# Kernel optimization log

Measured on AMD Instinct MI355X. Metric: run time of the kernel, lower is better.

The kernel has to match this reference:

```python
import jax, jax.numpy as jnp
import numpy as np

THRESH = 0.5
TAU = 0.5
GAMMA = 1.0
BETA = 0.9
A = 0.5
B = 0.5


def zif_spike(v):
    # ZIF surrogate: forward is hard threshold (v > 0).
    return (v > 0).astype(v.dtype)


def setup_inputs() -> dict:
    key = jax.random.key(0)
    x = jax.random.normal(key, (64, 8192, 100), dtype=jnp.float32)
    return {"x": x}


def reference(x):
    # x: [B, N, T]; scan over time with (mem, w) state kept per element.
    xt = jnp.moveaxis(x, 2, 0)  # [T, B, N]
    init_mem = jnp.zeros(xt.shape[1:], dtype=x.dtype)
    init_w = jnp.zeros(xt.shape[1:], dtype=x.dtype)

    def step(carry, x_t):
        mem, w = carry
        mem = mem * TAU + x_t - w
        spike = zif_spike(mem - THRESH)
        w = BETA * w + (1.0 - BETA) * (A * mem + B * spike)
        mem = mem - spike * THRESH  # soft reset
        return (mem, w), spike

    _, spikes = jax.lax.scan(step, (init_mem, init_w), xt)  # [T, B, N]
    return jnp.moveaxis(spikes, 0, 2)  # [B, N, T]
```

## Files before the change

### kernel.cpp

```cpp
#include <hip/hip_runtime.h>

#define T_STEPS 100
#define CHUNKS  25
#define TPB     64
#define ELEMS   64
#define PGRID   1536

typedef const __attribute__((address_space(1))) unsigned int g_u32;
typedef __attribute__((address_space(3))) unsigned int l_u32;

__global__ __launch_bounds__(TPB) void lif_kernel(const float* __restrict__ x,
                                                  float* __restrict__ out,
                                                  int nt) {
#pragma clang fp contract(off)
    __shared__ float4 tile[ELEMS * CHUNKS];

    const int lane = threadIdx.x;
    int ti = blockIdx.x;
    if (ti >= nt) return;

    {
        const float4* __restrict__ xb = (const float4*)x + (size_t)ti * (ELEMS * CHUNKS);
#pragma unroll
        for (int k = 0; k < CHUNKS; ++k) {
            __builtin_amdgcn_global_load_lds(
                (g_u32*)(xb + k * TPB + lane), (l_u32*)&tile[k * TPB], 16, 0, 0);
        }
    }
    asm volatile("s_waitcnt vmcnt(0)" ::: "memory");
    __builtin_amdgcn_sched_barrier(0);

    while (true) {
        float4 xv[CHUNKS];
#pragma unroll
        for (int c = 0; c < CHUNKS; ++c) xv[c] = tile[lane * CHUNKS + c];
        asm volatile("s_waitcnt lgkmcnt(0)" ::: "memory");
        __builtin_amdgcn_sched_barrier(0);

        const int nxt = ti + PGRID;
        if (nxt < nt) {
            const float4* __restrict__ xb = (const float4*)x + (size_t)nxt * (ELEMS * CHUNKS);
#pragma unroll
            for (int k = 0; k < CHUNKS; ++k) {
                __builtin_amdgcn_global_load_lds(
                    (g_u32*)(xb + k * TPB + lane), (l_u32*)&tile[k * TPB], 16, 0, 0);
            }
        }

        unsigned b0 = 0, b1 = 0, b2 = 0, b3 = 0;
        float mem = 0.0f, w = 0.0f;
#pragma unroll
        for (int c = 0; c < CHUNKS; ++c) {
            float xs[4] = {xv[c].x, xv[c].y, xv[c].z, xv[c].w};
#pragma unroll
            for (int j = 0; j < 4; ++j) {
                mem = (mem * 0.5f + xs[j]) - w;
                const bool fire = (mem - 0.5f) > 0.0f;
                const float spike = fire ? 1.0f : 0.0f;
                w = 0.9f * w + 0.1f * (0.5f * mem + 0.5f * spike);
                mem = mem - spike * 0.5f;
                const int t = c * 4 + j;
                const unsigned bit = fire ? 1u : 0u;
                if (t < 32)      b0 |= bit << t;
                else if (t < 64) b1 |= bit << (t - 32);
                else if (t < 96) b2 |= bit << (t - 64);
                else             b3 |= bit << (t - 96);
            }
        }

        float4* __restrict__ ob = (float4*)out + (size_t)ti * (ELEMS * CHUNKS);
#pragma unroll
        for (int k = 0; k < CHUNKS; ++k) {
            const int f = k * TPB + lane;
            const int e = f / 25;
            const int c = f - e * 25;
            const int a = e << 2;
            const unsigned w0 = (unsigned)__builtin_amdgcn_ds_bpermute(a, (int)b0);
            const unsigned w1 = (unsigned)__builtin_amdgcn_ds_bpermute(a, (int)b1);
            const unsigned w2 = (unsigned)__builtin_amdgcn_ds_bpermute(a, (int)b2);
            const unsigned w3 = (unsigned)__builtin_amdgcn_ds_bpermute(a, (int)b3);
            const unsigned word = (c < 16) ? ((c < 8) ? w0 : w1)
                                           : ((c < 24) ? w2 : w3);
            const int sh = (c & 7) * 4;
            float4 s;
            s.x = ((word >> (sh + 0)) & 1u) ? 1.0f : 0.0f;
            s.y = ((word >> (sh + 1)) & 1u) ? 1.0f : 0.0f;
            s.z = ((word >> (sh + 2)) & 1u) ? 1.0f : 0.0f;
            s.w = ((word >> (sh + 3)) & 1u) ? 1.0f : 0.0f;
            ob[f] = s;
        }

        ti = nxt;
        if (ti >= nt) break;
        asm volatile("s_waitcnt vmcnt(25)" ::: "memory");
        __builtin_amdgcn_sched_barrier(0);
    }
}

extern "C" void kernel_launch(void* const* d_in, const int* in_sizes, int n_in,
                              void* d_out, int out_size, void* d_ws, size_t ws_size,
                              hipStream_t stream) {
    const float* x = (const float*)d_in[0];
    float* out = (float*)d_out;
    int n_elem = in_sizes[0] / T_STEPS;
    int nt = n_elem / ELEMS;
    int grid = nt < PGRID ? nt : PGRID;

    lif_kernel<<<grid, TPB, 0, stream>>>(x, out, nt);
}
```

Before: 361.8 us.

## Switch to non-persistent 256-thread blocks with double-buffered time-slice loads

Replaces the persistent 64-thread grid, which prefetched whole 64-element tiles, with one 256-thread block per 256 elements. Each wave streams its 64 elements' time series in five 20-step slices through double-buffered LDS. The scan on one slice runs while the next slice loads, and LDS per block drops from a full tile to two small slice buffers. The cost is a much larger grid, no cross-tile prefetch, and strided 16-byte global gathers per slice instead of contiguous tile loads.

Measured after the change: 358.8 us. About the same (-0.8%).

```diff
diff --git a/kernel.cpp b/kernel.cpp
--- a/kernel.cpp
+++ b/kernel.cpp
@@ -2,64 +2,75 @@
 
 #define T_STEPS 100
 #define CHUNKS  25
-#define TPB     64
-#define ELEMS   64
-#define PGRID   1536
+#define TPB     256
+#define EPB     256
+#define SLICES  5
+#define SF4     5
+#define WSLOT   (64 * SF4)
 
 typedef const __attribute__((address_space(1))) unsigned int g_u32;
 typedef __attribute__((address_space(3))) unsigned int l_u32;
 
 __global__ __launch_bounds__(TPB) void lif_kernel(const float* __restrict__ x,
-                                                  float* __restrict__ out,
-                                                  int nt) {
+                                                  float* __restrict__ out) {
 #pragma clang fp contract(off)
-    __shared__ float4 tile[ELEMS * CHUNKS];
+    __shared__ float4 lds[2][EPB * SF4];
 
-    const int lane = threadIdx.x;
-    int ti = blockIdx.x;
-    if (ti >= nt) return;
+    const int tid  = threadIdx.x;
+    const int lane = tid & 63;
+    const int w    = tid >> 6;
 
-    {
-        const float4* __restrict__ xb = (const float4*)x + (size_t)ti * (ELEMS * CHUNKS);
+    const float* __restrict__ xw =
+        x + ((size_t)blockIdx.x * EPB + (size_t)w * 64) * T_STEPS;
+
+    const float* src[SF4];
 #pragma unroll
-        for (int k = 0; k < CHUNKS; ++k) {
-            __builtin_amdgcn_global_load_lds(
-                (g_u32*)(xb + k * TPB + lane), (l_u32*)&tile[k * TPB], 16, 0, 0);
+    for (int i = 0; i < SF4; ++i) {
+        const int f = i * 64 + lane;
+        const int e = f / SF4;
+        const int c = f - e * SF4;
+        src[i] = xw + e * T_STEPS + c * 4;
+    }
+
+#pragma unroll
+    for (int i = 0; i < SF4; ++i)
+        __builtin_amdgcn_global_load_lds(
+            (g_u32*)src[i], (l_u32*)&lds[0][w * WSLOT + i * 64], 16, 0, 0);
+
+    unsigned b0 = 0, b1 = 0, b2 = 0, b3 = 0;
+    float mem = 0.0f, wreg = 0.0f;
+
+#pragma unroll
+    for (int s = 0; s < SLICES; ++s) {
+        const int buf = s & 1;
+
+        if (s + 1 < SLICES) {
+#pragma unroll
+            for (int i = 0; i < SF4; ++i)
+                __builtin_amdgcn_global_load_lds(
+                    (g_u32*)(src[i] + (s + 1) * 4 * SF4),
+                    (l_u32*)&lds[buf ^ 1][w * WSLOT + i * 64], 16, 0, 0);
+            asm volatile("s_waitcnt vmcnt(5)" ::: "memory");
+        } else {
+            asm volatile("s_waitcnt vmcnt(0)" ::: "memory");
         }
-    }
-    asm volatile("s_waitcnt vmcnt(0)" ::: "memory");
-    __builtin_amdgcn_sched_barrier(0);
-
-    while (true) {
-        float4 xv[CHUNKS];
-#pragma unroll
-        for (int c = 0; c < CHUNKS; ++c) xv[c] = tile[lane * CHUNKS + c];
-        asm volatile("s_waitcnt lgkmcnt(0)" ::: "memory");
         __builtin_amdgcn_sched_barrier(0);
 
-        const int nxt = ti + PGRID;
-        if (nxt < nt) {
-            const float4* __restrict__ xb = (const float4*)x + (size_t)nxt * (ELEMS * CHUNKS);
+        float4 xv[SF4];
 #pragma unroll
-            for (int k = 0; k < CHUNKS; ++k) {
-                __builtin_amdgcn_global_load_lds(
-                    (g_u32*)(xb + k * TPB + lane), (l_u32*)&tile[k * TPB], 16, 0, 0);
-            }
-        }
+        for (int c = 0; c < SF4; ++c) xv[c] = lds[buf][tid * SF4 + c];
 
-        unsigned b0 = 0, b1 = 0, b2 = 0, b3 = 0;
-        float mem = 0.0f, w = 0.0f;
 #pragma unroll
-        for (int c = 0; c < CHUNKS; ++c) {
+        for (int c = 0; c < SF4; ++c) {
             float xs[4] = {xv[c].x, xv[c].y, xv[c].z, xv[c].w};
 #pragma unroll
             for (int j = 0; j < 4; ++j) {
-                mem = (mem * 0.5f + xs[j]) - w;
+                mem = (mem * 0.5f + xs[j]) - wreg;
                 const bool fire = (mem - 0.5f) > 0.0f;
                 const float spike = fire ? 1.0f : 0.0f;
-                w = 0.9f * w + 0.1f * (0.5f * mem + 0.5f * spike);
+                wreg = 0.9f * wreg + 0.1f * (0.5f * mem + 0.5f * spike);
                 mem = mem - spike * 0.5f;
-                const int t = c * 4 + j;
+                const int t = s * 20 + c * 4 + j;
                 const unsigned bit = fire ? 1u : 0u;
                 if (t < 32)      b0 |= bit << t;
                 else if (t < 64) b1 |= bit << (t - 32);
@@ -67,33 +78,29 @@
                 else             b3 |= bit << (t - 96);
             }
         }
+    }
 
-        float4* __restrict__ ob = (float4*)out + (size_t)ti * (ELEMS * CHUNKS);
+    float4* __restrict__ ow =
+        (float4*)out + ((size_t)blockIdx.x * EPB + (size_t)w * 64) * CHUNKS;
 #pragma unroll
-        for (int k = 0; k < CHUNKS; ++k) {
-            const int f = k * TPB + lane;
-            const int e = f / 25;
-            const int c = f - e * 25;
-            const int a = e << 2;
-            const unsigned w0 = (unsigned)__builtin_amdgcn_ds_bpermute(a, (int)b0);
-            const unsigned w1 = (unsigned)__builtin_amdgcn_ds_bpermute(a, (int)b1);
-            const unsigned w2 = (unsigned)__builtin_amdgcn_ds_bpermute(a, (int)b2);
-            const unsigned w3 = (unsigned)__builtin_amdgcn_ds_bpermute(a, (int)b3);
-            const unsigned word = (c < 16) ? ((c < 8) ? w0 : w1)
-                                           : ((c < 24) ? w2 : w3);
-            const int sh = (c & 7) * 4;
-            float4 s;
-            s.x = ((word >> (sh + 0)) & 1u) ? 1.0f : 0.0f;
-            s.y = ((word >> (sh + 1)) & 1u) ? 1.0f : 0.0f;
-            s.z = ((word >> (sh + 2)) & 1u) ? 1.0f : 0.0f;
-            s.w = ((word >> (sh + 3)) & 1u) ? 1.0f : 0.0f;
-            ob[f] = s;
-        }
-
-        ti = nxt;
-        if (ti >= nt) break;
-        asm volatile("s_waitcnt vmcnt(25)" ::: "memory");
-        __builtin_amdgcn_sched_barrier(0);
+    for (int k = 0; k < CHUNKS; ++k) {
+        const int f = k * 64 + lane;
+        const int e = f / 25;
+        const int c = f - e * 25;
+        const int a = e << 2;
+        const unsigned w0 = (unsigned)__builtin_amdgcn_ds_bpermute(a, (int)b0);
+        const unsigned w1 = (unsigned)__builtin_amdgcn_ds_bpermute(a, (int)b1);
+        const unsigned w2 = (unsigned)__builtin_amdgcn_ds_bpermute(a, (int)b2);
+        const unsigned w3 = (unsigned)__builtin_amdgcn_ds_bpermute(a, (int)b3);
+        const unsigned word = (c < 16) ? ((c < 8) ? w0 : w1)
+                                       : ((c < 24) ? w2 : w3);
+        const int sh = (c & 7) * 4;
+        float4 sv;
+        sv.x = ((word >> (sh + 0)) & 1u) ? 1.0f : 0.0f;
+        sv.y = ((word >> (sh + 1)) & 1u) ? 1.0f : 0.0f;
+        sv.z = ((word >> (sh + 2)) & 1u) ? 1.0f : 0.0f;
+        sv.w = ((word >> (sh + 3)) & 1u) ? 1.0f : 0.0f;
+        ow[f] = sv;
     }
 }
 
@@ -103,8 +110,7 @@
     const float* x = (const float*)d_in[0];
     float* out = (float*)d_out;
     int n_elem = in_sizes[0] / T_STEPS;
-    int nt = n_elem / ELEMS;
-    int grid = nt < PGRID ? nt : PGRID;
+    int grid = n_elem / EPB;
 
-    lif_kernel<<<grid, TPB, 0, stream>>>(x, out, nt);
+    lif_kernel<<<grid, TPB, 0, stream>>>(x, out);
 }
```

## Double-buffer LDS tiles and stream LDS reads inside the recurrence

Applied to the files above, without the earlier changes.

Replaces the single LDS tile with two buffers so the prefetch of the next tile can be issued before the current tile is consumed. LDS values are now read chunk by chunk inside the time loop instead of all 25 float4s being staged into registers first, which cuts register pressure. The persistent grid also grows from 1536 to 2048 blocks. In exchange, LDS use per block doubles, which may limit occupancy. The vmcnt(25) wait also relies on the output stores being counted as well.

Measured after the change: 365.8 us. About the same (+1.1%).

```diff
diff --git a/kernel.cpp b/kernel.cpp
--- a/kernel.cpp
+++ b/kernel.cpp
@@ -4,7 +4,8 @@
 #define CHUNKS  25
 #define TPB     64
 #define ELEMS   64
-#define PGRID   1536
+#define TILE_F4 (ELEMS * CHUNKS)
+#define GRID    2048
 
 typedef const __attribute__((address_space(1))) unsigned int g_u32;
 typedef __attribute__((address_space(3))) unsigned int l_u32;
@@ -13,68 +14,66 @@
                                                   float* __restrict__ out,
                                                   int nt) {
 #pragma clang fp contract(off)
-    __shared__ float4 tile[ELEMS * CHUNKS];
+    __shared__ float4 tile[2][TILE_F4];
 
     const int lane = threadIdx.x;
-    int ti = blockIdx.x;
-    if (ti >= nt) return;
+    int t = blockIdx.x;
+    if (t >= nt) return;
 
     {
-        const float4* __restrict__ xb = (const float4*)x + (size_t)ti * (ELEMS * CHUNKS);
+        const float4* __restrict__ xb = (const float4*)x + (size_t)t * TILE_F4;
 #pragma unroll
-        for (int k = 0; k < CHUNKS; ++k) {
+        for (int k = 0; k < CHUNKS; ++k)
             __builtin_amdgcn_global_load_lds(
-                (g_u32*)(xb + k * TPB + lane), (l_u32*)&tile[k * TPB], 16, 0, 0);
-        }
+                (g_u32*)(xb + k * TPB + lane), (l_u32*)&tile[0][k * TPB], 16, 0, 0);
     }
     asm volatile("s_waitcnt vmcnt(0)" ::: "memory");
     __builtin_amdgcn_sched_barrier(0);
 
+    int buf = 0;
     while (true) {
-        float4 xv[CHUNKS];
+        const int nxt = t + GRID;
+        const bool hn = nxt < nt;
+
+        if (hn) {
+            const float4* __restrict__ xb = (const float4*)x + (size_t)nxt * TILE_F4;
 #pragma unroll
-        for (int c = 0; c < CHUNKS; ++c) xv[c] = tile[lane * CHUNKS + c];
-        asm volatile("s_waitcnt lgkmcnt(0)" ::: "memory");
-        __builtin_amdgcn_sched_barrier(0);
+            for (int k = 0; k < CHUNKS; ++k)
+                __builtin_amdgcn_global_load_lds(
+                    (g_u32*)(xb + k * TPB + lane),
+                    (l_u32*)&tile[buf ^ 1][k * TPB], 16, 0, 0);
+        }
 
-        const int nxt = ti + PGRID;
-        if (nxt < nt) {
-            const float4* __restrict__ xb = (const float4*)x + (size_t)nxt * (ELEMS * CHUNKS);
+        unsigned b0 = 0, b1 = 0, b2 = 0, b3 = 0;
+        float mem = 0.0f, wreg = 0.0f;
+        const float4* tb = tile[buf];
 #pragma unroll
-            for (int k = 0; k < CHUNKS; ++k) {
-                __builtin_amdgcn_global_load_lds(
-                    (g_u32*)(xb + k * TPB + lane), (l_u32*)&tile[k * TPB], 16, 0, 0);
+        for (int c = 0; c < CHUNKS; ++c) {
+            const float4 xv = tb[lane * CHUNKS + c];
+            float xs[4] = {xv.x, xv.y, xv.z, xv.w};
+#pragma unroll
+            for (int j = 0; j < 4; ++j) {
+                mem = (mem * 0.5f + xs[j]) - wreg;
+                const bool fire = (mem - 0.5f) > 0.0f;
+                const float spike = fire ? 1.0f : 0.0f;
+                wreg = 0.9f * wreg + 0.1f * (0.5f * mem + 0.5f * spike);
+                mem = mem - spike * 0.5f;
+                const int tt = c * 4 + j;
+                const unsigned bit = fire ? 1u : 0u;
+                if (tt < 32)      b0 |= bit << tt;
+                else if (tt < 64) b1 |= bit << (tt - 32);
+                else if (tt < 96) b2 |= bit << (tt - 64);
+                else              b3 |= bit << (tt - 96);
             }
         }
 
-        unsigned b0 = 0, b1 = 0, b2 = 0, b3 = 0;
-        float mem = 0.0f, w = 0.0f;
-#pragma unroll
-        for (int c = 0; c < CHUNKS; ++c) {
-            float xs[4] = {xv[c].x, xv[c].y, xv[c].z, xv[c].w};
-#pragma unroll
-            for (int j = 0; j < 4; ++j) {
-                mem = (mem * 0.5f + xs[j]) - w;
-                const bool fire = (mem - 0.5f) > 0.0f;
-                const float spike = fire ? 1.0f : 0.0f;
-                w = 0.9f * w + 0.1f * (0.5f * mem + 0.5f * spike);
-                mem = mem - spike * 0.5f;
-                const int t = c * 4 + j;
-                const unsigned bit = fire ? 1u : 0u;
-                if (t < 32)      b0 |= bit << t;
-                else if (t < 64) b1 |= bit << (t - 32);
-                else if (t < 96) b2 |= bit << (t - 64);
-                else             b3 |= bit << (t - 96);
-            }
-        }
-
-        float4* __restrict__ ob = (float4*)out + (size_t)ti * (ELEMS * CHUNKS);
+        float4* __restrict__ ob = (float4*)out + (size_t)t * TILE_F4;
 #pragma unroll
         for (int k = 0; k < CHUNKS; ++k) {
-            const int f = k * TPB + lane;
-            const int e = f / 25;
-            const int c = f - e * 25;
-            const int a = e << 2;
+            const int f  = k * TPB + lane;
+            const int el = f / 25;
+            const int c  = f - el * 25;
+            const int a  = el << 2;
             const unsigned w0 = (unsigned)__builtin_amdgcn_ds_bpermute(a, (int)b0);
             const unsigned w1 = (unsigned)__builtin_amdgcn_ds_bpermute(a, (int)b1);
             const unsigned w2 = (unsigned)__builtin_amdgcn_ds_bpermute(a, (int)b2);
@@ -82,18 +81,19 @@
             const unsigned word = (c < 16) ? ((c < 8) ? w0 : w1)
                                            : ((c < 24) ? w2 : w3);
             const int sh = (c & 7) * 4;
-            float4 s;
-            s.x = ((word >> (sh + 0)) & 1u) ? 1.0f : 0.0f;
-            s.y = ((word >> (sh + 1)) & 1u) ? 1.0f : 0.0f;
-            s.z = ((word >> (sh + 2)) & 1u) ? 1.0f : 0.0f;
-            s.w = ((word >> (sh + 3)) & 1u) ? 1.0f : 0.0f;
-            ob[f] = s;
+            float4 sv;
+            sv.x = ((word >> (sh + 0)) & 1u) ? 1.0f : 0.0f;
+            sv.y = ((word >> (sh + 1)) & 1u) ? 1.0f : 0.0f;
+            sv.z = ((word >> (sh + 2)) & 1u) ? 1.0f : 0.0f;
+            sv.w = ((word >> (sh + 3)) & 1u) ? 1.0f : 0.0f;
+            ob[f] = sv;
         }
 
-        ti = nxt;
-        if (ti >= nt) break;
+        if (!hn) break;
         asm volatile("s_waitcnt vmcnt(25)" ::: "memory");
         __builtin_amdgcn_sched_barrier(0);
+        buf ^= 1;
+        t = nxt;
     }
 }
 
@@ -104,7 +104,7 @@
     float* out = (float*)d_out;
     int n_elem = in_sizes[0] / T_STEPS;
     int nt = n_elem / ELEMS;
-    int grid = nt < PGRID ? nt : PGRID;
+    int grid = nt < GRID ? nt : GRID;
 
     lif_kernel<<<grid, TPB, 0, stream>>>(x, out, nt);
 }
```
